# Performance work log

Hardware: AMD Instinct MI355X
Metric: run time of the kernel (lower is better)

## Reference

```python
import jax, jax.numpy as jnp
import numpy as np

R, D, H, NLAYERS = 128, 64, 64, 3
B, N = 64, 1024
INIT_W = 0.1


def setup_inputs() -> dict:
    key = jax.random.key(0)
    ks = jax.random.split(key, 10)
    x = jax.random.normal(ks[0], (B, D, N), dtype=jnp.float32)
    L = jax.random.randint(ks[1], (B, 1, N), 0, 2, dtype=jnp.int32)
    wq0 = INIT_W * jax.random.normal(ks[2], (R, D), dtype=jnp.float32)
    wqr = INIT_W * jax.random.normal(ks[3], (NLAYERS - 1, R, R), dtype=jnp.float32)
    wk0 = INIT_W * jax.random.normal(ks[4], (R, D), dtype=jnp.float32)
    wkr = INIT_W * jax.random.normal(ks[5], (NLAYERS - 1, R, R), dtype=jnp.float32)
    wv0 = INIT_W * jax.random.normal(ks[6], (R, D), dtype=jnp.float32)
    wvr = INIT_W * jax.random.normal(ks[7], (NLAYERS - 1, R, R), dtype=jnp.float32)
    wor = INIT_W * jax.random.normal(ks[8], (NLAYERS - 1, R, R), dtype=jnp.float32)
    wo_last = INIT_W * jax.random.normal(ks[9], (H, R), dtype=jnp.float32)
    return {"x": x, "L": L, "wq0": wq0, "wqr": wqr, "wk0": wk0, "wkr": wkr,
            "wv0": wv0, "wvr": wvr, "wor": wor, "wo_last": wo_last}


def reference(x, L, wq0, wqr, wk0, wkr, wv0, wvr, wor, wo_last):
    # x: [B, d, N]; L: [B, 1, N] neighbor mask (first row used)
    Lrow = L[:, 0, :].astype(jnp.float32)                      # [B, N]
    num_neighbors = jnp.sum((Lrow >= 1).astype(jnp.float32), axis=1)[:, None, None] + 1.0  # [B,1,1]
    scale = jnp.sqrt(num_neighbors)
    mask = Lrow[:, None, :]                                    # [B, 1, N], broadcast over r

    inp = x
    for layer in range(NLAYERS):
        Wq = wq0 if layer == 0 else wqr[layer - 1]
        Wk = wk0 if layer == 0 else wkr[layer - 1]
        Wv = wv0 if layer == 0 else wvr[layer - 1]
        # sigmoid-gated projections: [B, r, N]
        Q = jax.nn.sigmoid(jnp.einsum('rd,bdn->brn', Wq, inp))
        K = jax.nn.sigmoid(jnp.einsum('rd,bdn->brn', Wk, inp))
        V = jax.nn.sigmoid(jnp.einsum('rd,bdn->brn', Wv, inp))
        # degree-scaled softmax attention over agents: scores [B, N, N]
        A = jax.nn.softmax(jnp.einsum('brn,brm->bnm', Q, K) / scale, axis=-1)
        # o[b,r,n] = sum_m A[b,n,m] * V[b,r,m]  -> [B, r, N]
        o = jnp.einsum('bnm,brm->brn', A, V)
        Wo = wor[layer] if layer < NLAYERS - 1 else wo_last
        inp = jax.nn.silu(jnp.einsum('or,brn->bon', Wo, o))
        if layer != NLAYERS - 1:  # remask_bias=True
            inp = mask * inp
    return inp  # [B, h, N]
```

## Files before the change

kernel.cpp:

```cpp
#include <hip/hip_runtime.h>


typedef __bf16 bf16;
typedef bf16 bf16x2 __attribute__((ext_vector_type(2)));
typedef bf16 bf16x4 __attribute__((ext_vector_type(4)));
typedef bf16 bf16x8 __attribute__((ext_vector_type(8)));
typedef float f32x4 __attribute__((ext_vector_type(4)));
typedef float f32x16 __attribute__((ext_vector_type(16)));

#define MFMA32(a, b, c) __builtin_amdgcn_mfma_f32_32x32x16_bf16(a, b, c, 0, 0, 0)
#define ZERO16 {0,0,0,0,0,0,0,0,0,0,0,0,0,0,0,0}
#define LOG2E 1.44269504f

__device__ __forceinline__ float fast_sigmoid(float x) {
  return __builtin_amdgcn_rcpf(1.0f + exp2f(-LOG2E * x));
}

__global__ __launch_bounds__(256) void prep_kernel(
    const int* __restrict__ L,
    const float* __restrict__ wq0, const float* __restrict__ wqr,
    const float* __restrict__ wk0, const float* __restrict__ wkr,
    const float* __restrict__ wv0, const float* __restrict__ wvr,
    const float* __restrict__ wor, const float* __restrict__ wo_last,
    float* __restrict__ scale_inv, float* __restrict__ biasv,
    bf16* __restrict__ wbf) {
  __shared__ int red[256];
  const int blk = blockIdx.x;
  const int tid = threadIdx.x;
  if (blk < 64) {
    int cnt = 0;
    for (int n = tid; n < 1024; n += 256) cnt += (L[blk * 1024 + n] >= 1) ? 1 : 0;
    red[tid] = cnt;
    __syncthreads();
    for (int s = 128; s > 0; s >>= 1) {
      if (tid < s) red[tid] += red[tid + s];
      __syncthreads();
    }
    if (tid == 0) {
      float iv = rsqrtf((float)red[0] + 1.0f);
      scale_inv[blk] = iv;
      biasv[blk] = fmaxf(0.0f, 128.0f * iv * LOG2E - 80.0f);
    }
  } else {
    for (int i = (blk - 64) * 256 + tid; i < 163840; i += 64 * 256) {
      float v;
      if      (i <   8192) v = wq0[i];
      else if (i <  40960) v = wqr[i - 8192];
      else if (i <  49152) v = wk0[i - 40960];
      else if (i <  81920) v = wkr[i - 49152];
      else if (i <  90112) v = wv0[i - 81920];
      else if (i < 122880) v = wvr[i - 90112];
      else if (i < 155648) v = wor[i - 122880];
      else                 v = wo_last[i - 155648];
      wbf[i] = (bf16)v;
    }
  }
}

__global__ __launch_bounds__(256) void xk0_kernel(
    const float* __restrict__ x, const bf16* __restrict__ Wk,
    const bf16* __restrict__ Wv, bf16* __restrict__ xT,
    bf16* __restrict__ Kt, bf16* __restrict__ Vn) {
  __shared__ float tile[64][65];
  __shared__ __attribute__((aligned(16))) bf16 inp_lds[64 * 72];
  const int tid = threadIdx.x;
  const int lane = tid & 63, wv = tid >> 6;
  const int la = lane & 31, hi = lane >> 5;
  const int b = blockIdx.x >> 4;
  const int t0 = (blockIdx.x & 15) * 64;

  {
    const int nl = tid & 63, dbase = (tid >> 6) * 16;
#pragma unroll
    for (int i = 0; i < 16; i++) {
      int d = dbase + i;
      tile[d][nl] = x[(size_t)(b * 64 + d) * 1024 + t0 + nl];
    }
  }
  __syncthreads();
  {
    const int dl = (tid & 31) * 2, nb = (tid >> 5) * 8;
#pragma unroll
    for (int i = 0; i < 8; i++) {
      int n = nb + i;
      bf16x2 pr = {(bf16)tile[dl][n], (bf16)tile[dl + 1][n]};
      *(bf16x2*)(xT + (size_t)(b * 1024 + t0 + n) * 64 + dl) = pr;
      *(bf16x2*)&inp_lds[n * 72 + dl] = pr;
    }
  }
  __syncthreads();

  const int sub = wv & 1;
  if (wv < 2) {
#pragma unroll
    for (int rt2 = 0; rt2 < 2; rt2++) {
      const int rt = 2 * sub + rt2;
      bf16x8 wf[4];
#pragma unroll
      for (int ks = 0; ks < 4; ks++)
        wf[ks] = *(const bf16x8*)(Wk + (size_t)(la + 32 * rt) * 64 + hi * 8 + ks * 16);
#pragma unroll
      for (int tt = 0; tt < 2; tt++) {
        f32x16 acc = ZERO16;
#pragma unroll
        for (int ks = 0; ks < 4; ks++) {
          bf16x8 bfr = *(const bf16x8*)&inp_lds[(la + 32 * tt) * 72 + hi * 8 + ks * 16];
          acc = MFMA32(wf[ks], bfr, acc);
        }
#pragma unroll
        for (int g = 0; g < 4; g++) {
          bf16x4 pk;
#pragma unroll
          for (int i = 0; i < 4; i++) pk[i] = (bf16)fast_sigmoid(acc[4 * g + i]);
          *(bf16x4*)(Kt + (size_t)(b * 1024 + t0 + 32 * tt + la) * 128 +
                     32 * rt + 8 * g + 4 * hi) = pk;
        }
      }
    }
  } else {
#pragma unroll
    for (int rc2 = 0; rc2 < 2; rc2++) {
      const int rc = 2 * sub + rc2;
      bf16x8 wf[4];
#pragma unroll
      for (int ks = 0; ks < 4; ks++)
        wf[ks] = *(const bf16x8*)(Wv + (size_t)(la + 32 * rc) * 64 + hi * 8 + ks * 16);
#pragma unroll
      for (int tt = 0; tt < 2; tt++) {
        f32x16 acc = ZERO16;
#pragma unroll
        for (int ks = 0; ks < 4; ks++) {
          bf16x8 afr = *(const bf16x8*)&inp_lds[(la + 32 * tt) * 72 + hi * 8 + ks * 16];
          acc = MFMA32(afr, wf[ks], acc);
        }
#pragma unroll
        for (int g = 0; g < 4; g++) {
          bf16x4 pk;
#pragma unroll
          for (int i = 0; i < 4; i++) pk[i] = (bf16)fast_sigmoid(acc[4 * g + i]);
          *(bf16x4*)(Vn + (size_t)(b * 128 + la + 32 * rc) * 1024 +
                     t0 + 32 * tt + 8 * g + 4 * hi) = pk;
        }
      }
    }
  }
}

template <int DIN>
__global__ __launch_bounds__(256) void kv_kernel(
    const bf16* __restrict__ inpT, const bf16* __restrict__ Wk,
    const bf16* __restrict__ Wv, bf16* __restrict__ Kt,
    bf16* __restrict__ Vn) {
  constexpr int SIN = DIN + 8;
  constexpr int KS = DIN / 16;
  constexpr int CPR = DIN / 8;
  __shared__ __attribute__((aligned(16))) bf16 inp_lds[64 * SIN];
  const int tid = threadIdx.x;
  const int lane = tid & 63, wv = tid >> 6;
  const int la = lane & 31, hi = lane >> 5;
  const int b = blockIdx.x >> 4;
  const int t0 = (blockIdx.x & 15) * 64;

  for (int i = tid; i < 64 * CPR; i += 256) {
    int row = i / CPR, c = i % CPR;
    *(bf16x8*)&inp_lds[row * SIN + c * 8] =
        *(const bf16x8*)(inpT + (size_t)(b * 1024 + t0 + row) * DIN + c * 8);
  }
  __syncthreads();

  const int sub = wv & 1;
  if (wv < 2) {
#pragma unroll
    for (int rt2 = 0; rt2 < 2; rt2++) {
      const int rt = 2 * sub + rt2;
      bf16x8 wf[KS];
#pragma unroll
      for (int ks = 0; ks < KS; ks++)
        wf[ks] = *(const bf16x8*)(Wk + (size_t)(la + 32 * rt) * DIN + hi * 8 + ks * 16);
#pragma unroll
      for (int tt = 0; tt < 2; tt++) {
        f32x16 acc = ZERO16;
#pragma unroll
        for (int ks = 0; ks < KS; ks++) {
          bf16x8 bfr = *(const bf16x8*)&inp_lds[(la + 32 * tt) * SIN + hi * 8 + ks * 16];
          acc = MFMA32(wf[ks], bfr, acc);
        }
#pragma unroll
        for (int g = 0; g < 4; g++) {
          bf16x4 pk;
#pragma unroll
          for (int i = 0; i < 4; i++) pk[i] = (bf16)fast_sigmoid(acc[4 * g + i]);
          *(bf16x4*)(Kt + (size_t)(b * 1024 + t0 + 32 * tt + la) * 128 +
                     32 * rt + 8 * g + 4 * hi) = pk;
        }
      }
    }
  } else {
#pragma unroll
    for (int rc2 = 0; rc2 < 2; rc2++) {
      const int rc = 2 * sub + rc2;
      bf16x8 wf[KS];
#pragma unroll
      for (int ks = 0; ks < KS; ks++)
        wf[ks] = *(const bf16x8*)(Wv + (size_t)(la + 32 * rc) * DIN + hi * 8 + ks * 16);
#pragma unroll
      for (int tt = 0; tt < 2; tt++) {
        f32x16 acc = ZERO16;
#pragma unroll
        for (int ks = 0; ks < KS; ks++) {
          bf16x8 afr = *(const bf16x8*)&inp_lds[(la + 32 * tt) * SIN + hi * 8 + ks * 16];
          acc = MFMA32(afr, wf[ks], acc);
        }
#pragma unroll
        for (int g = 0; g < 4; g++) {
          bf16x4 pk;
#pragma unroll
          for (int i = 0; i < 4; i++) pk[i] = (bf16)fast_sigmoid(acc[4 * g + i]);
          *(bf16x4*)(Vn + (size_t)(b * 128 + la + 32 * rc) * 1024 +
                     t0 + 32 * tt + 8 * g + 4 * hi) = pk;
        }
      }
    }
  }
}

template <int DIN>
__global__ __launch_bounds__(256, 2) void flash_kernel(
    const bf16* __restrict__ inpT, const bf16* __restrict__ Wq,
    const bf16* __restrict__ Kt, const bf16* __restrict__ Vn,
    const float* __restrict__ scale_inv, const float* __restrict__ biasv,
    const int* __restrict__ L, const bf16* __restrict__ Wo,
    void* __restrict__ outp, int last,
    const bf16* __restrict__ Wkn, const bf16* __restrict__ Wvn,
    bf16* __restrict__ Ktn, bf16* __restrict__ Vnn, int kvgen) {
  __shared__ __attribute__((aligned(16))) char smem[70656];
  bf16* K_lds = (bf16*)smem;
  bf16* V_lds = (bf16*)(smem + 17408);
  bf16* P_lds = (bf16*)(smem + 35840);

  const int tid = threadIdx.x;
  const int lane = tid & 63, wv = tid >> 6;
  const int la = lane & 31, hi = lane >> 5;
  const int b = blockIdx.x >> 3;
  const int q0 = (blockIdx.x & 7) * 128;

  const float inv2 = scale_inv[b] * LOG2E;
  const float bb = biasv[b];

  {
    constexpr int SIN = DIN + 8;
    constexpr int KSD = DIN / 16;
    constexpr int CPR = DIN / 8;
    bf16* inp_s = (bf16*)smem;
    for (int i = tid; i < 128 * CPR; i += 256) {
      int row = i / CPR, c = i % CPR;
      *(bf16x8*)&inp_s[row * SIN + c * 8] =
          *(const bf16x8*)(inpT + (size_t)(b * 1024 + q0 + row) * DIN + c * 8);
    }
    __syncthreads();
    bf16* Q_lds = (bf16*)(smem + 35840);
    bf16x8 wf[KSD];
#pragma unroll
    for (int ks = 0; ks < KSD; ks++)
      wf[ks] = *(const bf16x8*)(Wq + (size_t)(la + 32 * wv) * DIN + hi * 8 + ks * 16);
#pragma unroll
    for (int nt = 0; nt < 4; nt++) {
      f32x16 acc = ZERO16;
#pragma unroll
      for (int ks = 0; ks < KSD; ks++) {
        bf16x8 bfr = *(const bf16x8*)&inp_s[(la + 32 * nt) * SIN + hi * 8 + ks * 16];
        acc = MFMA32(wf[ks], bfr, acc);
      }
#pragma unroll
      for (int g = 0; g < 4; g++) {
        bf16x4 pk;
#pragma unroll
        for (int i = 0; i < 4; i++)
          pk[i] = (bf16)(fast_sigmoid(acc[4 * g + i]) * inv2);
        *(bf16x4*)&Q_lds[(size_t)(32 * nt + la) * 136 + 32 * wv + 8 * g + 4 * hi] = pk;
      }
    }
    __syncthreads();
  }

  const int ms = wv & 1, nw = wv >> 1;
  bf16x8 qB[2][8];
#pragma unroll
  for (int nt = 0; nt < 2; nt++)
#pragma unroll
    for (int ks = 0; ks < 8; ks++)
      qB[nt][ks] = *(const bf16x8*)((bf16*)(smem + 35840) +
                                    (size_t)(64 * nw + 32 * nt + la) * 136 +
                                    hi * 8 + ks * 16);

  const int krow = tid >> 4, kc = (tid & 15) * 8;
  const int vrow = tid >> 3, vc = (tid & 7) * 8;
  const bf16* kbase = Kt + (size_t)b * 1024 * 128;
  const bf16* vbase = Vn + (size_t)b * 128 * 1024;
  bf16x8 kr[4], vr[4];
#pragma unroll
  for (int p = 0; p < 4; p++) {
    kr[p] = *(const bf16x8*)(kbase + (size_t)(krow + 16 * p) * 128 + kc);
    vr[p] = *(const bf16x8*)(vbase + (size_t)(vrow + 32 * p) * 1024 + vc);
  }

  const int nh = wv & 1, rh = wv >> 1;
  f32x16 acc_o[2][2] = {{ZERO16, ZERO16}, {ZERO16, ZERO16}};
  float rs[2] = {0.f, 0.f};

  for (int it = 0; it < 16; it++) {
    __syncthreads();
#pragma unroll
    for (int p = 0; p < 4; p++)
      *(bf16x8*)&K_lds[(krow + 16 * p) * 136 + kc] = kr[p];
#pragma unroll
    for (int p = 0; p < 4; p++)
      *(bf16x8*)&V_lds[(vrow + 32 * p) * 72 + vc] = vr[p];
    __syncthreads();

    if (it < 15) {
      const int m1 = (it + 1) * 64;
#pragma unroll
      for (int p = 0; p < 4; p++) {
        kr[p] = *(const bf16x8*)(kbase + (size_t)(m1 + krow + 16 * p) * 128 + kc);
        vr[p] = *(const bf16x8*)(vbase + (size_t)(vrow + 32 * p) * 1024 + m1 + vc);
      }
    }

    bf16x8 kf[8];
#pragma unroll
    for (int ks = 0; ks < 8; ks++)
      kf[ks] = *(const bf16x8*)&K_lds[(32 * ms + la) * 136 + hi * 8 + ks * 16];
#pragma unroll
    for (int nt = 0; nt < 2; nt++) {
      f32x16 sa = ZERO16;
#pragma unroll
      for (int ks = 0; ks < 8; ks++) sa = MFMA32(kf[ks], qB[nt][ks], sa);
#pragma unroll
      for (int g = 0; g < 4; g++) {
        bf16x4 pk;
#pragma unroll
        for (int i = 0; i < 4; i++) {
          float p = exp2f(sa[4 * g + i] - bb);
          rs[nt] += p;
          pk[i] = (bf16)p;
        }
        *(bf16x4*)&P_lds[(size_t)(64 * nw + 32 * nt + la) * 72 +
                         32 * ms + 8 * g + 4 * hi] = pk;
      }
    }
    __syncthreads();

    bf16x8 pA[2][4];
#pragma unroll
    for (int nt2 = 0; nt2 < 2; nt2++)
#pragma unroll
      for (int k2 = 0; k2 < 4; k2++)
        pA[nt2][k2] = *(const bf16x8*)&P_lds[(size_t)(64 * nh + 32 * nt2 + la) * 72 +
                                             hi * 8 + k2 * 16];
#pragma unroll
    for (int rt = 0; rt < 2; rt++) {
#pragma unroll
      for (int k2 = 0; k2 < 4; k2++) {
        bf16x8 vB = *(const bf16x8*)&V_lds[(size_t)(64 * rh + 32 * rt + la) * 72 +
                                           hi * 8 + k2 * 16];
        acc_o[0][rt] = MFMA32(pA[0][k2], vB, acc_o[0][rt]);
        acc_o[1][rt] = MFMA32(pA[1][k2], vB, acc_o[1][rt]);
      }
    }
  }

  rs[0] += __shfl_xor(rs[0], 32, 64);
  rs[1] += __shfl_xor(rs[1], 32, 64);
  __syncthreads();
  float* rsp = (float*)smem;
  if (lane < 32) {
    rsp[ms * 128 + 64 * nw + la] = rs[0];
    rsp[ms * 128 + 64 * nw + 32 + la] = rs[1];
  }
  __syncthreads();

  bf16* O_lds = (bf16*)(smem + 35840);
#pragma unroll
  for (int nt2 = 0; nt2 < 2; nt2++) {
#pragma unroll
    for (int g = 0; g < 4; g++) {
      const int nb = 64 * nh + 32 * nt2 + 8 * g + 4 * hi;
      f32x4 ra = *(f32x4*)&rsp[nb];
      f32x4 rc = *(f32x4*)&rsp[128 + nb];
      f32x4 is;
#pragma unroll
      for (int i = 0; i < 4; i++) is[i] = 1.0f / (ra[i] + rc[i]);
#pragma unroll
      for (int rt = 0; rt < 2; rt++) {
#pragma unroll
        for (int i = 0; i < 4; i++) {
          O_lds[(size_t)(nb + i) * 136 + 64 * rh + 32 * rt + la] =
              (bf16)(acc_o[nt2][rt][4 * g + i] * is[i]);
        }
      }
    }
  }
  __syncthreads();

  if (!last) {
    bf16* out_b = (bf16*)outp;
    bf16* O2 = (bf16*)smem;
    const int* Lg = L + b * 1024 + q0;
    bf16x8 wB[8];
#pragma unroll
    for (int ks = 0; ks < 8; ks++)
      wB[ks] = *(const bf16x8*)(Wo + (size_t)(la + 32 * wv) * 128 + hi * 8 + ks * 16);
#pragma unroll
    for (int nt = 0; nt < 4; nt++) {
      f32x16 acc = ZERO16;
#pragma unroll
      for (int ks = 0; ks < 8; ks++) {
        bf16x8 oA = *(const bf16x8*)&O_lds[(size_t)(la + 32 * nt) * 136 +
                                           hi * 8 + ks * 16];
        acc = MFMA32(oA, wB[ks], acc);
      }
#pragma unroll
      for (int g = 0; g < 4; g++) {
#pragma unroll
        for (int i = 0; i < 4; i++) {
          int n = 32 * nt + 8 * g + 4 * hi + i;
          float xv = acc[4 * g + i];
          float y = xv * fast_sigmoid(xv) * (float)Lg[n];
          out_b[(size_t)(b * 1024 + q0 + n) * 128 + 32 * wv + la] = (bf16)y;
          if (kvgen) O2[(size_t)n * 136 + 32 * wv + la] = (bf16)y;
        }
      }
    }
    if (kvgen) {
      __syncthreads();
      const int sub = wv & 1;
      const bf16* W2 = (wv < 2) ? Wkn : Wvn;
#pragma unroll
      for (int rt2 = 0; rt2 < 2; rt2++) {
        const int rt = 2 * sub + rt2;
        bf16x8 wf[8];
#pragma unroll
        for (int ks = 0; ks < 8; ks++)
          wf[ks] = *(const bf16x8*)(W2 + (size_t)(la + 32 * rt) * 128 +
                                    hi * 8 + ks * 16);
#pragma unroll
        for (int tt = 0; tt < 4; tt++) {
          f32x16 acc = ZERO16;
          if (wv < 2) {
#pragma unroll
            for (int ks = 0; ks < 8; ks++) {
              bf16x8 bB = *(const bf16x8*)&O2[(size_t)(32 * tt + la) * 136 +
                                              hi * 8 + ks * 16];
              acc = MFMA32(wf[ks], bB, acc);
            }
#pragma unroll
            for (int g = 0; g < 4; g++) {
              bf16x4 pk;
#pragma unroll
              for (int i = 0; i < 4; i++) pk[i] = (bf16)fast_sigmoid(acc[4 * g + i]);
              *(bf16x4*)(Ktn + (size_t)(b * 1024 + q0 + 32 * tt + la) * 128 +
                         32 * rt + 8 * g + 4 * hi) = pk;
            }
          } else {
#pragma unroll
            for (int ks = 0; ks < 8; ks++) {
              bf16x8 aA = *(const bf16x8*)&O2[(size_t)(32 * tt + la) * 136 +
                                              hi * 8 + ks * 16];
              acc = MFMA32(aA, wf[ks], acc);
            }
#pragma unroll
            for (int g = 0; g < 4; g++) {
              bf16x4 pk;
#pragma unroll
              for (int i = 0; i < 4; i++) pk[i] = (bf16)fast_sigmoid(acc[4 * g + i]);
              *(bf16x4*)(Vnn + (size_t)(b * 128 + 32 * rt + la) * 1024 +
                         q0 + 32 * tt + 8 * g + 4 * hi) = pk;
            }
          }
        }
      }
    }
  } else {
    const int hs = wv & 1, nq = wv >> 1;
    float* outf = (float*)outp;
    bf16x8 wA[8];
#pragma unroll
    for (int ks = 0; ks < 8; ks++)
      wA[ks] = *(const bf16x8*)(Wo + (size_t)(la + 32 * hs) * 128 + hi * 8 + ks * 16);
#pragma unroll
    for (int t = 0; t < 2; t++) {
      const int ns4 = nq + 2 * t;
      f32x16 acc = ZERO16;
#pragma unroll
      for (int ks = 0; ks < 8; ks++) {
        bf16x8 oB = *(const bf16x8*)&O_lds[(size_t)(32 * ns4 + la) * 136 +
                                           hi * 8 + ks * 16];
        acc = MFMA32(wA[ks], oB, acc);
      }
#pragma unroll
      for (int g = 0; g < 4; g++) {
#pragma unroll
        for (int i = 0; i < 4; i++) {
          int h = 32 * hs + 8 * g + 4 * hi + i;
          float xv = acc[4 * g + i];
          outf[(size_t)(b * 64 + h) * 1024 + q0 + 32 * ns4 + la] =
              xv * fast_sigmoid(xv);
        }
      }
    }
  }
}

__global__ __launch_bounds__(256) void xpose_kernel(const float* __restrict__ x,
                                                    bf16* __restrict__ xT) {
  __shared__ float tile[64][65];
  const int blk = blockIdx.x;
  const int b = blk >> 4;
  const int n0 = (blk & 15) * 64;
  const int tid = threadIdx.x;
  {
    const int nl = tid & 63, dbase = (tid >> 6) * 16;
#pragma unroll
    for (int i = 0; i < 16; i++) {
      int d = dbase + i;
      tile[d][nl] = x[(size_t)(b * 64 + d) * 1024 + n0 + nl];
    }
  }
  __syncthreads();
  {
    const int dl = (tid & 31) * 2, nb = (tid >> 5) * 8;
#pragma unroll
    for (int i = 0; i < 8; i++) {
      int n = nb + i;
      bf16x2 pr = {(bf16)tile[dl][n], (bf16)tile[dl + 1][n]};
      *(bf16x2*)(xT + (size_t)(b * 1024 + n0 + n) * 64 + dl) = pr;
    }
  }
}

extern "C" void kernel_launch(void* const* d_in, const int* in_sizes, int n_in,
                              void* d_out, int out_size, void* d_ws, size_t ws_size,
                              hipStream_t stream) {
  const float* x = (const float*)d_in[0];
  const int* L = (const int*)d_in[1];
  const float* wq0 = (const float*)d_in[2];
  const float* wqr = (const float*)d_in[3];
  const float* wk0 = (const float*)d_in[4];
  const float* wkr = (const float*)d_in[5];
  const float* wv0 = (const float*)d_in[6];
  const float* wvr = (const float*)d_in[7];
  const float* wor = (const float*)d_in[8];
  const float* wo_last = (const float*)d_in[9];

  char* ws = (char*)d_ws;
  float* scale_inv = (float*)(ws + 0);
  float* biasv = (float*)(ws + 1024);
  bf16* wbf = (bf16*)(ws + 4096);
  bf16* xT = (bf16*)(ws + 335872);
  bf16* inpT = (bf16*)(ws + 8724480);
  bf16* KtA = (bf16*)(ws + 25501696);
  bf16* VnA = (bf16*)(ws + 42278912);
  bf16* KtB = (bf16*)(ws + 59056128);
  bf16* VnB = (bf16*)(ws + 75833344);

  prep_kernel<<<128, 256, 0, stream>>>(L, wq0, wqr, wk0, wkr, wv0, wvr, wor,
                                       wo_last, scale_inv, biasv, wbf);

  if (ws_size >= 92610560) {
    xk0_kernel<<<1024, 256, 0, stream>>>(x, wbf + 40960, wbf + 81920, xT, KtA, VnA);
    flash_kernel<64><<<512, 256, 0, stream>>>(
        xT, wbf + 0, KtA, VnA, scale_inv, biasv, L, wbf + 122880, (void*)inpT, 0,
        wbf + 49152, wbf + 90112, KtB, VnB, 1);
    flash_kernel<128><<<512, 256, 0, stream>>>(
        inpT, wbf + 8192, KtB, VnB, scale_inv, biasv, L, wbf + 139264,
        (void*)inpT, 0, wbf + 65536, wbf + 106496, KtA, VnA, 1);
    flash_kernel<128><<<512, 256, 0, stream>>>(
        inpT, wbf + 24576, KtA, VnA, scale_inv, biasv, L, wbf + 155648, d_out, 1,
        nullptr, nullptr, nullptr, nullptr, 0);
  } else if (ws_size >= 59056128) {
    xpose_kernel<<<1024, 256, 0, stream>>>(x, xT);
    for (int l = 0; l < 3; l++) {
      const bf16* Wq = (l == 0) ? wbf + 0 : wbf + 8192 + (size_t)(l - 1) * 16384;
      const bf16* Wk = (l == 0) ? wbf + 40960 : wbf + 49152 + (size_t)(l - 1) * 16384;
      const bf16* Wv = (l == 0) ? wbf + 81920 : wbf + 90112 + (size_t)(l - 1) * 16384;
      const bf16* Wo = (l < 2) ? wbf + 122880 + (size_t)l * 16384 : wbf + 155648;
      void* outp = (l < 2) ? (void*)inpT : (void*)d_out;
      if (l == 0) {
        kv_kernel<64><<<1024, 256, 0, stream>>>(xT, Wk, Wv, KtA, VnA);
        flash_kernel<64><<<512, 256, 0, stream>>>(xT, Wq, KtA, VnA, scale_inv,
                                                  biasv, L, Wo, outp, 0,
                                                  nullptr, nullptr, nullptr,
                                                  nullptr, 0);
      } else {
        kv_kernel<128><<<1024, 256, 0, stream>>>(inpT, Wk, Wv, KtA, VnA);
        flash_kernel<128><<<512, 256, 0, stream>>>(inpT, Wq, KtA, VnA, scale_inv,
                                                   biasv, L, Wo, outp,
                                                   (l == 2) ? 1 : 0, nullptr,
                                                   nullptr, nullptr, nullptr, 0);
      }
    }
  }
}
```

Baseline: 324.2 us.

## Keep Q and P in registers via lane shuffles and double-buffer K/V tiles

Restructures the flash attention loop so each wave owns 32 query rows end to end. The Q projection and softmax probabilities are converted into MFMA operand layout with cross-half-wave shuffles rather than round-tripping through LDS. K/V tiles are double-buffered in shared memory, leaving one barrier per iteration, and padding strides shrink so LDS drops to about 67KB. The cross-wave row-sum reduction goes away, but each wave now reads the full K/V tile and holds more accumulator registers, which risks register pressure at two blocks per SM.

```diff
diff --git a/kernel.cpp b/kernel.cpp
--- a/kernel.cpp
+++ b/kernel.cpp
@@ -14,6 +14,19 @@
 
 __device__ __forceinline__ float fast_sigmoid(float x) {
   return __builtin_amdgcn_rcpf(1.0f + exp2f(-LOG2E * x));
+}
+
+__device__ __forceinline__ bf16x4 shfl_xor32_b4(bf16x4 v) {
+  union { bf16x4 h; int u[2]; } a;
+  a.h = v;
+  a.u[0] = __shfl_xor(a.u[0], 32, 64);
+  a.u[1] = __shfl_xor(a.u[1], 32, 64);
+  return a.h;
+}
+__device__ __forceinline__ bf16x8 cat44(bf16x4 lo, bf16x4 hi4) {
+  union { bf16x8 o; bf16x4 p[2]; } u;
+  u.p[0] = lo; u.p[1] = hi4;
+  return u.o;
 }
 
 __global__ __launch_bounds__(256) void prep_kernel(
@@ -233,10 +246,7 @@
     void* __restrict__ outp, int last,
     const bf16* __restrict__ Wkn, const bf16* __restrict__ Wvn,
     bf16* __restrict__ Ktn, bf16* __restrict__ Vnn, int kvgen) {
-  __shared__ __attribute__((aligned(16))) char smem[70656];
-  bf16* K_lds = (bf16*)smem;
-  bf16* V_lds = (bf16*)(smem + 17408);
-  bf16* P_lds = (bf16*)(smem + 35840);
+  __shared__ __attribute__((aligned(16))) bf16 smem[34304];
 
   const int tid = threadIdx.x;
   const int lane = tid & 63, wv = tid >> 6;
@@ -249,49 +259,14 @@
 
   {
     constexpr int SIN = DIN + 8;
-    constexpr int KSD = DIN / 16;
     constexpr int CPR = DIN / 8;
-    bf16* inp_s = (bf16*)smem;
     for (int i = tid; i < 128 * CPR; i += 256) {
       int row = i / CPR, c = i % CPR;
-      *(bf16x8*)&inp_s[row * SIN + c * 8] =
+      *(bf16x8*)&smem[row * SIN + c * 8] =
           *(const bf16x8*)(inpT + (size_t)(b * 1024 + q0 + row) * DIN + c * 8);
     }
-    __syncthreads();
-    bf16* Q_lds = (bf16*)(smem + 35840);
-    bf16x8 wf[KSD];
-#pragma unroll
-    for (int ks = 0; ks < KSD; ks++)
-      wf[ks] = *(const bf16x8*)(Wq + (size_t)(la + 32 * wv) * DIN + hi * 8 + ks * 16);
-#pragma unroll
-    for (int nt = 0; nt < 4; nt++) {
-      f32x16 acc = ZERO16;
-#pragma unroll
-      for (int ks = 0; ks < KSD; ks++) {
-        bf16x8 bfr = *(const bf16x8*)&inp_s[(la + 32 * nt) * SIN + hi * 8 + ks * 16];
-        acc = MFMA32(wf[ks], bfr, acc);
-      }
-#pragma unroll
-      for (int g = 0; g < 4; g++) {
-        bf16x4 pk;
-#pragma unroll
-        for (int i = 0; i < 4; i++)
-          pk[i] = (bf16)(fast_sigmoid(acc[4 * g + i]) * inv2);
-        *(bf16x4*)&Q_lds[(size_t)(32 * nt + la) * 136 + 32 * wv + 8 * g + 4 * hi] = pk;
-      }
-    }
-    __syncthreads();
-  }
-
-  const int ms = wv & 1, nw = wv >> 1;
-  bf16x8 qB[2][8];
-#pragma unroll
-  for (int nt = 0; nt < 2; nt++)
-#pragma unroll
-    for (int ks = 0; ks < 8; ks++)
-      qB[nt][ks] = *(const bf16x8*)((bf16*)(smem + 35840) +
-                                    (size_t)(64 * nw + 32 * nt + la) * 136 +
-                                    hi * 8 + ks * 16);
+  }
+  __syncthreads();
 
   const int krow = tid >> 4, kc = (tid & 15) * 8;
   const int vrow = tid >> 3, vc = (tid & 7) * 8;
@@ -304,20 +279,91 @@
     vr[p] = *(const bf16x8*)(vbase + (size_t)(vrow + 32 * p) * 1024 + vc);
   }
 
-  const int nh = wv & 1, rh = wv >> 1;
-  f32x16 acc_o[2][2] = {{ZERO16, ZERO16}, {ZERO16, ZERO16}};
-  float rs[2] = {0.f, 0.f};
+  bf16x8 qB[8];
+  {
+    constexpr int SIN = DIN + 8;
+    constexpr int KSD = DIN / 16;
+    bf16x8 ib[KSD];
+#pragma unroll
+    for (int ks = 0; ks < KSD; ks++)
+      ib[ks] = *(const bf16x8*)&smem[(32 * wv + la) * SIN + hi * 8 + ks * 16];
+#pragma unroll
+    for (int rq = 0; rq < 4; rq++) {
+      f32x16 acc = ZERO16;
+#pragma unroll
+      for (int ks = 0; ks < KSD; ks++) {
+        bf16x8 wf = *(const bf16x8*)(Wq + (size_t)(32 * rq + la) * DIN +
+                                     hi * 8 + ks * 16);
+        acc = MFMA32(wf, ib[ks], acc);
+      }
+      bf16x4 pg[4];
+#pragma unroll
+      for (int g = 0; g < 4; g++)
+#pragma unroll
+        for (int i = 0; i < 4; i++)
+          pg[g][i] = (bf16)(fast_sigmoid(acc[4 * g + i]) * inv2);
+#pragma unroll
+      for (int s = 0; s < 2; s++) {
+        bf16x4 mine = hi ? pg[2 * s + 1] : pg[2 * s];
+        bf16x4 send = hi ? pg[2 * s] : pg[2 * s + 1];
+        bf16x4 recv = shfl_xor32_b4(send);
+        qB[2 * rq + s] = hi ? cat44(recv, mine) : cat44(mine, recv);
+      }
+    }
+  }
+  __syncthreads();
+
+  f32x16 acc_o[4] = {ZERO16, ZERO16, ZERO16, ZERO16};
+  float rs = 0.f;
+
+  auto computeT = [&](int koff, int voff) {
+    const bf16* Ks = smem + koff;
+    const bf16* Vs = smem + voff;
+    bf16x8 pf[4];
+#pragma unroll
+    for (int mt = 0; mt < 2; mt++) {
+      f32x16 sa = ZERO16;
+#pragma unroll
+      for (int ks = 0; ks < 8; ks++) {
+        bf16x8 kf = *(const bf16x8*)&Ks[(32 * mt + la) * 132 + hi * 8 + ks * 16];
+        sa = MFMA32(kf, qB[ks], sa);
+      }
+      bf16x4 pg[4];
+#pragma unroll
+      for (int g = 0; g < 4; g++)
+#pragma unroll
+        for (int i = 0; i < 4; i++) {
+          float p = exp2f(sa[4 * g + i] - bb);
+          rs += p;
+          pg[g][i] = (bf16)p;
+        }
+#pragma unroll
+      for (int s = 0; s < 2; s++) {
+        bf16x4 mine = hi ? pg[2 * s + 1] : pg[2 * s];
+        bf16x4 send = hi ? pg[2 * s] : pg[2 * s + 1];
+        bf16x4 recv = shfl_xor32_b4(send);
+        pf[2 * mt + s] = hi ? cat44(recv, mine) : cat44(mine, recv);
+      }
+    }
+#pragma unroll
+    for (int rt = 0; rt < 4; rt++)
+#pragma unroll
+      for (int k2 = 0; k2 < 4; k2++) {
+        bf16x8 vB = *(const bf16x8*)&Vs[(32 * rt + la) * 68 + hi * 8 + k2 * 16];
+        acc_o[rt] = MFMA32(pf[k2], vB, acc_o[rt]);
+      }
+  };
 
   for (int it = 0; it < 16; it++) {
-    __syncthreads();
+    const int wb2 = it & 1;
+    bf16* Kw = smem + wb2 * 8448;
+    bf16* Vw = smem + 16896 + wb2 * 8704;
 #pragma unroll
     for (int p = 0; p < 4; p++)
-      *(bf16x8*)&K_lds[(krow + 16 * p) * 136 + kc] = kr[p];
+      *(bf16x8*)&Kw[(krow + 16 * p) * 132 + kc] = kr[p];
 #pragma unroll
     for (int p = 0; p < 4; p++)
-      *(bf16x8*)&V_lds[(vrow + 32 * p) * 72 + vc] = vr[p];
-    __syncthreads();
-
+      *(bf16x8*)&Vw[(vrow + 32 * p) * 68 + vc] = vr[p];
     if (it < 15) {
       const int m1 = (it + 1) * 64;
 #pragma unroll
@@ -326,114 +372,64 @@
         vr[p] = *(const bf16x8*)(vbase + (size_t)(vrow + 32 * p) * 1024 + m1 + vc);
       }
     }
-
-    bf16x8 kf[8];
-#pragma unroll
-    for (int ks = 0; ks < 8; ks++)
-      kf[ks] = *(const bf16x8*)&K_lds[(32 * ms + la) * 136 + hi * 8 + ks * 16];
-#pragma unroll
-    for (int nt = 0; nt < 2; nt++) {
-      f32x16 sa = ZERO16;
-#pragma unroll
-      for (int ks = 0; ks < 8; ks++) sa = MFMA32(kf[ks], qB[nt][ks], sa);
-#pragma unroll
-      for (int g = 0; g < 4; g++) {
-        bf16x4 pk;
-#pragma unroll
-        for (int i = 0; i < 4; i++) {
-          float p = exp2f(sa[4 * g + i] - bb);
-          rs[nt] += p;
-          pk[i] = (bf16)p;
-        }
-        *(bf16x4*)&P_lds[(size_t)(64 * nw + 32 * nt + la) * 72 +
-                         32 * ms + 8 * g + 4 * hi] = pk;
-      }
-    }
+    if (it > 0) computeT((wb2 ^ 1) * 8448, 16896 + (wb2 ^ 1) * 8704);
     __syncthreads();
-
-    bf16x8 pA[2][4];
-#pragma unroll
-    for (int nt2 = 0; nt2 < 2; nt2++)
-#pragma unroll
-      for (int k2 = 0; k2 < 4; k2++)
-        pA[nt2][k2] = *(const bf16x8*)&P_lds[(size_t)(64 * nh + 32 * nt2 + la) * 72 +
-                                             hi * 8 + k2 * 16];
-#pragma unroll
-    for (int rt = 0; rt < 2; rt++) {
-#pragma unroll
-      for (int k2 = 0; k2 < 4; k2++) {
-        bf16x8 vB = *(const bf16x8*)&V_lds[(size_t)(64 * rh + 32 * rt + la) * 72 +
-                                           hi * 8 + k2 * 16];
-        acc_o[0][rt] = MFMA32(pA[0][k2], vB, acc_o[0][rt]);
-        acc_o[1][rt] = MFMA32(pA[1][k2], vB, acc_o[1][rt]);
-      }
-    }
-  }
-
-  rs[0] += __shfl_xor(rs[0], 32, 64);
-  rs[1] += __shfl_xor(rs[1], 32, 64);
-  __syncthreads();
-  float* rsp = (float*)smem;
-  if (lane < 32) {
-    rsp[ms * 128 + 64 * nw + la] = rs[0];
-    rsp[ms * 128 + 64 * nw + 32 + la] = rs[1];
-  }
-  __syncthreads();
-
-  bf16* O_lds = (bf16*)(smem + 35840);
-#pragma unroll
-  for (int nt2 = 0; nt2 < 2; nt2++) {
-#pragma unroll
-    for (int g = 0; g < 4; g++) {
-      const int nb = 64 * nh + 32 * nt2 + 8 * g + 4 * hi;
-      f32x4 ra = *(f32x4*)&rsp[nb];
-      f32x4 rc = *(f32x4*)&rsp[128 + nb];
-      f32x4 is;
-#pragma unroll
-      for (int i = 0; i < 4; i++) is[i] = 1.0f / (ra[i] + rc[i]);
-#pragma unroll
-      for (int rt = 0; rt < 2; rt++) {
-#pragma unroll
-        for (int i = 0; i < 4; i++) {
-          O_lds[(size_t)(nb + i) * 136 + 64 * rh + 32 * rt + la] =
-              (bf16)(acc_o[nt2][rt][4 * g + i] * is[i]);
-        }
-      }
+  }
+  computeT(8448, 25600);
+
+  float rsf = rs + __shfl_xor(rs, 32, 64);
+  __syncthreads();
+  bf16* O_lds = smem;
+#pragma unroll
+  for (int g = 0; g < 4; g++) {
+#pragma unroll
+    for (int i = 0; i < 4; i++) {
+      float is = 1.0f / __shfl(rsf, 8 * g + 4 * hi + i, 64);
+      const int nrow = 32 * wv + 8 * g + 4 * hi + i;
+#pragma unroll
+      for (int rt = 0; rt < 4; rt++)
+        O_lds[(size_t)nrow * 132 + 32 * rt + la] =
+            (bf16)(acc_o[rt][4 * g + i] * is);
     }
   }
   __syncthreads();
 
   if (!last) {
     bf16* out_b = (bf16*)outp;
-    bf16* O2 = (bf16*)smem;
     const int* Lg = L + b * 1024 + q0;
     bf16x8 wB[8];
 #pragma unroll
     for (int ks = 0; ks < 8; ks++)
       wB[ks] = *(const bf16x8*)(Wo + (size_t)(la + 32 * wv) * 128 + hi * 8 + ks * 16);
+    f32x16 accp[4];
 #pragma unroll
     for (int nt = 0; nt < 4; nt++) {
-      f32x16 acc = ZERO16;
+      accp[nt] = ZERO16;
 #pragma unroll
       for (int ks = 0; ks < 8; ks++) {
-        bf16x8 oA = *(const bf16x8*)&O_lds[(size_t)(la + 32 * nt) * 136 +
+        bf16x8 oA = *(const bf16x8*)&O_lds[(size_t)(la + 32 * nt) * 132 +
                                            hi * 8 + ks * 16];
-        acc = MFMA32(oA, wB[ks], acc);
-      }
+        accp[nt] = MFMA32(oA, wB[ks], accp[nt]);
+      }
+    }
+    if (kvgen) __syncthreads();
+#pragma unroll
+    for (int nt = 0; nt < 4; nt++) {
 #pragma unroll
       for (int g = 0; g < 4; g++) {
 #pragma unroll
         for (int i = 0; i < 4; i++) {
           int n = 32 * nt + 8 * g + 4 * hi + i;
-          float xv = acc[4 * g + i];
+          float xv = accp[nt][4 * g + i];
           float y = xv * fast_sigmoid(xv) * (float)Lg[n];
           out_b[(size_t)(b * 1024 + q0 + n) * 128 + 32 * wv + la] = (bf16)y;
-          if (kvgen) O2[(size_t)n * 136 + 32 * wv + la] = (bf16)y;
+          if (kvgen) O_lds[(size_t)n * 132 + 32 * wv + la] = (bf16)y;
         }
       }
     }
     if (kvgen) {
       __syncthreads();
+      const bf16* O2 = O_lds;
       const int sub = wv & 1;
       const bf16* W2 = (wv < 2) ? Wkn : Wvn;
 #pragma unroll
@@ -450,7 +446,7 @@
           if (wv < 2) {
 #pragma unroll
             for (int ks = 0; ks < 8; ks++) {
-              bf16x8 bB = *(const bf16x8*)&O2[(size_t)(32 * tt + la) * 136 +
+              bf16x8 bB = *(const bf16x8*)&O2[(size_t)(32 * tt + la) * 132 +
                                               hi * 8 + ks * 16];
               acc = MFMA32(wf[ks], bB, acc);
             }
@@ -465,7 +461,7 @@
           } else {
 #pragma unroll
             for (int ks = 0; ks < 8; ks++) {
-              bf16x8 aA = *(const bf16x8*)&O2[(size_t)(32 * tt + la) * 136 +
+              bf16x8 aA = *(const bf16x8*)&O2[(size_t)(32 * tt + la) * 132 +
                                               hi * 8 + ks * 16];
               acc = MFMA32(aA, wf[ks], acc);
             }
@@ -494,7 +490,7 @@
       f32x16 acc = ZERO16;
 #pragma unroll
       for (int ks = 0; ks < 8; ks++) {
-        bf16x8 oB = *(const bf16x8*)&O_lds[(size_t)(32 * ns4 + la) * 136 +
+        bf16x8 oB = *(const bf16x8*)&O_lds[(size_t)(32 * ns4 + la) * 132 +
                                            hi * 8 + ks * 16];
         acc = MFMA32(wA[ks], oB, acc);
       }
```

Result: slower. 602.2 us (+85.7%).
